# Performance work log

Hardware: AMD Instinct MI355X
Metric: run time of the kernel (lower is better)

Reference implementation:

```python
import jax, jax.numpy as jnp
import numpy as np

B, NQ, NA, C, L = 8, 2048, 64, 128, 4  # batches, queries/mol, atoms/mol, hidden, num_layers
CUTOFF = 8.0
E_AQ, E_QQ = 131072, 262144


def _ln(x, g, b):
    m = x.mean(-1, keepdims=True)
    v = ((x - m) ** 2).mean(-1, keepdims=True)
    return (x - m) * jax.lax.rsqrt(v + 1e-5) * g + b


def _egnn(p, h_src, h_tgt, pos_src, pos_tgt, t_emb, esrc, etgt):
    (mW1, mb1, mW2, mb2, cW1, cb1, cW2, cb2, nW1, nb1, nW2, nb2, g, b) = p
    rel = pos_tgt[etgt] - pos_src[esrc]                      # (E,3)
    sq = (rel ** 2).sum(-1, keepdims=True)                   # (E,1)
    mi = jnp.concatenate([h_src[esrc], h_tgt[etgt], sq, t_emb[etgt]], -1)  # (E,3C+1)
    msg = jax.nn.silu(jax.nn.silu(mi @ mW1 + mb1) @ mW2 + mb2)             # (E,C)
    w = jnp.tanh(jax.nn.silu(msg @ cW1 + cb1) @ cW2 + cb2)                 # (E,1)
    vel = jnp.zeros_like(pos_tgt).at[etgt].add(w * rel)
    agg = jnp.zeros_like(h_tgt).at[etgt].add(msg)
    u = jnp.concatenate([h_tgt, agg], -1)
    h_new = _ln(h_tgt + (jax.nn.silu(u @ nW1 + nb1) @ nW2 + nb2), g, b)
    return h_new, vel


def setup_inputs() -> dict:
    key = jax.random.key(0)
    ks = iter(jax.random.split(key, 64))
    n = lambda shape, s=0.05: jax.random.normal(next(ks), shape, dtype=jnp.float32) * s
    NQT, NAT = B * NQ, B * NA
    return dict(
        x_t=jax.random.normal(next(ks), (NQT, 3), dtype=jnp.float32) * 3.0,
        t_query=jax.random.uniform(next(ks), (NQT,), dtype=jnp.float32),
        atom_pos=jax.random.normal(next(ks), (NAT, 3), dtype=jnp.float32) * 3.0,
        atom_feat=n((NAT, 256), 1.0),
        edge_aq_src=jax.random.randint(next(ks), (E_AQ,), 0, NAT, dtype=jnp.int32),
        edge_aq_tgt=jax.random.randint(next(ks), (E_AQ,), 0, NQT, dtype=jnp.int32),
        edge_qq_src=jax.random.randint(next(ks), (E_QQ,), 0, NQT, dtype=jnp.int32),
        edge_qq_tgt=jax.random.randint(next(ks), (E_QQ,), 0, NQT, dtype=jnp.int32),
        atom_proj_W=n((256, C)), atom_proj_b=jnp.zeros((C,)),
        time_W1=n((C, 4 * C)), time_b1=jnp.zeros((4 * C,)),
        time_W2=n((4 * C, C)), time_b2=jnp.zeros((C,)),
        qi_W1=n((1, C)), qi_b1=jnp.zeros((C,)),
        qi_W2=n((C, C)), qi_b2=jnp.zeros((C,)),
        msg_W1=n((2 * L, 3 * C + 1, 2 * C)), msg_b1=jnp.zeros((2 * L, 2 * C)),
        msg_W2=n((2 * L, 2 * C, C)), msg_b2=jnp.zeros((2 * L, C)),
        cw_W1=n((2 * L, C, C // 2)), cw_b1=jnp.zeros((2 * L, C // 2)),
        cw_W2=n((2 * L, C // 2, 1)), cw_b2=jnp.zeros((2 * L, 1)),
        nu_W1=n((2 * L, 2 * C, C)), nu_b1=jnp.zeros((2 * L, C)),
        nu_W2=n((2 * L, C, C)), nu_b2=jnp.zeros((2 * L, C)),
        ln_g=jnp.ones((2 * L, C)), ln_b=jnp.zeros((2 * L, C)),
        vo_W1=n((C, C)), vo_b1=jnp.zeros((C,)),
        vo_W2=n((C, 1)), vo_b2=jnp.zeros((1,)),
    )


def reference(x_t, t_query, atom_pos, atom_feat,
              edge_aq_src, edge_aq_tgt, edge_qq_src, edge_qq_tgt,
              atom_proj_W, atom_proj_b,
              time_W1, time_b1, time_W2, time_b2,
              qi_W1, qi_b1, qi_W2, qi_b2,
              msg_W1, msg_b1, msg_W2, msg_b2,
              cw_W1, cw_b1, cw_W2, cw_b2,
              nu_W1, nu_b1, nu_W2, nu_b2,
              ln_g, ln_b,
              vo_W1, vo_b1, vo_W2, vo_b2):
    # atom features (no condition drop: eval mode)
    h_atom = atom_feat @ atom_proj_W + atom_proj_b

    # sinusoidal time embedding per query node
    half = C // 2
    freqs = jnp.exp(-np.log(10000.0) * jnp.arange(half, dtype=jnp.float32) / (half - 1))
    args = t_query[:, None] * freqs[None, :]
    emb = jnp.concatenate([jnp.sin(args), jnp.cos(args)], -1)
    t_emb = jax.nn.silu(emb @ time_W1 + time_b1) @ time_W2 + time_b2

    # init query features: log1p(mean_dist / cutoff), equal-size batches
    q = x_t.reshape(B, NQ, 3)
    a = atom_pos.reshape(B, NA, 3)
    sq = ((q[:, :, None, :] - a[:, None, :, :]) ** 2).sum(-1)  # (B,NQ,NA)
    log_dist = jnp.log1p(jnp.sqrt(sq.mean(-1)) / CUTOFF).reshape(-1, 1)
    h = jax.nn.silu(log_dist @ qi_W1 + qi_b1) @ qi_W2 + qi_b2

    layers = (msg_W1, msg_b1, msg_W2, msg_b2, cw_W1, cw_b1, cw_W2, cw_b2,
              nu_W1, nu_b1, nu_W2, nu_b2, ln_g, ln_b)
    pick = lambda j: tuple(arr[j] for arr in layers)

    vel = jnp.zeros_like(x_t)
    for i in range(L):
        h, dv = _egnn(pick(2 * i), h_atom, h, atom_pos, x_t, t_emb, edge_aq_src, edge_aq_tgt)
        vel = vel + dv
        h, dv = _egnn(pick(2 * i + 1), h, h, x_t, x_t, t_emb, edge_qq_src, edge_qq_tgt)
        vel = vel + dv

    scale = jax.nn.silu(h @ vo_W1 + vo_b1) @ vo_W2 + vo_b2   # (N_q,1)
    return vel * scale
```

## Files before the change

### kernel.cpp

```cpp
#include <hip/hip_runtime.h>

#define NQT 16384
#define NAT 512
#define EAQ 131072
#define EQQ 262144

typedef short short8 __attribute__((ext_vector_type(8)));
typedef float float4v __attribute__((ext_vector_type(4)));

__device__ __forceinline__ float silu_f(float x){ return x / (1.f + __expf(-x)); }

__device__ __forceinline__ short f2bf(float f){
  union { float f; unsigned u; } v; v.f = f;
  unsigned r = v.u + 0x7fff + ((v.u >> 16) & 1);
  return (short)(r >> 16);
}
__device__ __forceinline__ float bf2f(short s){
  union { unsigned u; float f; } v;
  v.u = ((unsigned)(unsigned short)s) << 16;
  return v.f;
}

__global__ __launch_bounds__(256) void k_hist2(
    const int* __restrict__ ta, const int* __restrict__ tq,
    int* __restrict__ ha, int* __restrict__ hq)
{
  int i = blockIdx.x*256 + threadIdx.x;
  atomicAdd(&hq[tq[i]], 1);
  if (i < EAQ) atomicAdd(&ha[ta[i]], 1);
}

__global__ __launch_bounds__(256) void k_scan2(int* __restrict__ ha, int* __restrict__ hq)
{
  int* hist = (blockIdx.x == 0) ? ha : hq;
  __shared__ int part[256];
  int t = threadIdx.x;
  int base = t * 64;
  int s = 0;
  for (int i = 0; i < 64; i++) s += hist[base + i];
  part[t] = s;
  __syncthreads();
  for (int off = 1; off < 256; off <<= 1){
    int v = (t >= off) ? part[t - off] : 0;
    __syncthreads();
    part[t] += v;
    __syncthreads();
  }
  int run = (t == 0) ? 0 : part[t-1];
  for (int i = 0; i < 64; i++){
    int h = hist[base + i];
    hist[base + i] = run;
    run += h;
  }
}

__global__ __launch_bounds__(256) void k_place2(
    const int* __restrict__ sa, const int* __restrict__ ta,
    const int* __restrict__ sq, const int* __restrict__ tq,
    int* __restrict__ ca, int* __restrict__ cq,
    int2* __restrict__ da, int2* __restrict__ dq)
{
  int i = blockIdx.x*256 + threadIdx.x;
  { int tg = tq[i]; int pos = atomicAdd(&cq[tg], 1); dq[pos] = make_int2(sq[i], tg); }
  if (i < EAQ){ int tg = ta[i]; int pos = atomicAdd(&ca[tg], 1); da[pos] = make_int2(sa[i], tg); }
}

__device__ __forceinline__ void pack_one(
    const float* __restrict__ W, short* __restrict__ out,
    int rows, int cols, int ksteps, int ntiles, int idx, int mode)
{
  int l8   = idx & 7;
  int lane = (idx >> 3) & 63;
  int kk   = (idx >> 9) % ksteps;
  int nt   = ((idx >> 9) / ksteps) % ntiles;
  int j    = idx / (512 * ksteps * ntiles);
  int k = kk*32 + (lane >> 4)*8 + l8;
  if (mode == 1) k += (k >= 256);
  else if (mode == 2) k = (k < 128) ? k + 128 : k + 129;
  int n = nt*16 + (lane & 15);
  out[idx] = f2bf(W[(size_t)j*rows*cols + (size_t)k*cols + n]);
}

__global__ __launch_bounds__(256) void k_packall(
    const float* __restrict__ mW1, const float* __restrict__ mW2,
    const float* __restrict__ cW1, const float* __restrict__ nW1,
    const float* __restrict__ nW2, const float* __restrict__ tW1,
    const float* __restrict__ tW2,
    short* W1ap, short* W1bcp, short* W2p, short* W3p,
    short* nW1p, short* nW2p, short* tW1p, short* tW2p)
{
  int b = blockIdx.x, t = threadIdx.x;
  if (b < 1024){ pack_one(mW1, W1ap, 385,256,4,16, b*256+t, 0); return; } b -= 1024;
  if (b < 2048){ pack_one(mW1, W1bcp,385,256,8,16, b*256+t, 2); return; } b -= 2048;
  if (b < 1024){ pack_one(mW2, W2p,  256,128,8, 8, b*256+t, 0); return; } b -= 1024;
  if (b <  256){ pack_one(cW1, W3p,  128, 64,4, 4, b*256+t, 0); return; } b -=  256;
  if (b < 1024){ pack_one(nW1, nW1p, 256,128,8, 8, b*256+t, 0); return; } b -= 1024;
  if (b <  512){ pack_one(nW2, nW2p, 128,128,4, 8, b*256+t, 0); return; } b -=  512;
  if (b <  256){ pack_one(tW1, tW1p, 128,512,4,32, b*256+t, 0); return; } b -=  256;
  pack_one(tW2, tW2p, 512,128,16,8, b*256+t, 0);
}

__global__ __launch_bounds__(256) void k_pre0(
    const float* __restrict__ hA, const float* __restrict__ temb,
    const float* __restrict__ mb1_0, const short* __restrict__ W1bcp0,
    const float* __restrict__ h_atom, const short* __restrict__ W1ap_base,
    short* __restrict__ Ptgt, short* __restrict__ psrc_aq)
{
  int t = threadIdx.x;
  int lane = t & 63, w = t >> 6;
  int mrow = lane & 15, quad = lane >> 4;
  int b = blockIdx.x;

  if (b < NQT/64){
    int m0 = b*64 + w*16;
    short8 areg[8];
    #pragma unroll
    for (int kk = 0; kk < 8; kk++){
      int k = kk*32 + quad*8;
      const float* bp = (kk >= 4) ? (temb + (size_t)(m0+mrow)*128 + (k - 128))
                                  : (hA   + (size_t)(m0+mrow)*128 + k);
      float4 f0 = *(const float4*)(bp);
      float4 f1 = *(const float4*)(bp + 4);
      short8 s;
      s[0]=f2bf(f0.x); s[1]=f2bf(f0.y); s[2]=f2bf(f0.z); s[3]=f2bf(f0.w);
      s[4]=f2bf(f1.x); s[5]=f2bf(f1.y); s[6]=f2bf(f1.z); s[7]=f2bf(f1.w);
      areg[kk] = s;
    }
    #pragma unroll
    for (int nt = 0; nt < 16; nt++){
      float4v acc = {0.f,0.f,0.f,0.f};
      const short8* Bb = (const short8*)(W1bcp0 + ((size_t)nt*8)*512 + lane*8);
      #pragma unroll
      for (int kk = 0; kk < 8; kk++)
        acc = __builtin_amdgcn_mfma_f32_16x16x32_bf16(areg[kk], Bb[kk*64], acc, 0, 0, 0);
      float bv = mb1_0[nt*16 + mrow];
      #pragma unroll
      for (int r = 0; r < 4; r++)
        Ptgt[(size_t)(m0 + quad*4 + r)*256 + nt*16 + mrow] = f2bf(acc[r] + bv);
    }
  } else {
    int bb = b - NQT/64;
    int idx = bb >> 3;
    int m0 = (bb & 7)*64 + w*16;
    const short* Wp = W1ap_base + (size_t)(2*idx)*32768;
    short8 areg[4];
    #pragma unroll
    for (int kk = 0; kk < 4; kk++){
      const float* bp = h_atom + (size_t)(m0+mrow)*128 + kk*32 + quad*8;
      float4 f0 = *(const float4*)(bp);
      float4 f1 = *(const float4*)(bp + 4);
      short8 s;
      s[0]=f2bf(f0.x); s[1]=f2bf(f0.y); s[2]=f2bf(f0.z); s[3]=f2bf(f0.w);
      s[4]=f2bf(f1.x); s[5]=f2bf(f1.y); s[6]=f2bf(f1.z); s[7]=f2bf(f1.w);
      areg[kk] = s;
    }
    #pragma unroll
    for (int nt = 0; nt < 16; nt++){
      float4v acc = {0.f,0.f,0.f,0.f};
      const short8* Bb = (const short8*)(Wp + ((size_t)nt*4)*512 + lane*8);
      #pragma unroll
      for (int kk = 0; kk < 4; kk++)
        acc = __builtin_amdgcn_mfma_f32_16x16x32_bf16(areg[kk], Bb[kk*64], acc, 0, 0, 0);
      #pragma unroll
      for (int r = 0; r < 4; r++)
        psrc_aq[(size_t)idx*131072 + (size_t)(m0 + quad*4 + r)*256 + nt*16 + mrow] = f2bf(acc[r]);
    }
  }
}

__global__ __launch_bounds__(128) void k_hatom(
    const float* __restrict__ feat, const float* __restrict__ W,
    const float* __restrict__ b, float* __restrict__ out)
{
  __shared__ float sf[256];
  int n = blockIdx.x, t = threadIdx.x;
  sf[t]       = feat[n*256 + t];
  sf[t + 128] = feat[n*256 + 128 + t];
  __syncthreads();
  float acc = b[t];
  for (int k = 0; k < 256; k++) acc += sf[k] * W[k*128 + t];
  out[n*128 + t] = acc;
}

__global__ __launch_bounds__(256) void k_temb(
    const float* __restrict__ tq,
    const short* __restrict__ W1p, const float* __restrict__ b1,
    const short* __restrict__ W2p, const float* __restrict__ b2,
    float* __restrict__ temb)
{
  __shared__ __align__(16) short A[32*136];
  __shared__ __align__(16) short B[32*528];
  int t = threadIdx.x;
  int n0 = blockIdx.x * 32;

  {
    int row = t >> 3, l = t & 7;
    float tv = tq[n0 + row];
    short* o = A + row*136;
    #pragma unroll
    for (int i = 0; i < 16; i++){
      int k = l*16 + i;
      int h = k & 63;
      float freq = __expf(-9.210340371976184f * (float)h * (1.f/63.f));
      float a = tv * freq;
      float v = (k < 64) ? __sinf(a) : __cosf(a);
      o[k] = f2bf(v);
    }
  }
  __syncthreads();

  int lane = t & 63, w = t >> 6;
  int mrow = lane & 15, quad = lane >> 4;

  for (int nti = 0; nti < 8; nti++){
    int nt = w*8 + nti;
    #pragma unroll
    for (int mt = 0; mt < 2; mt++){
      float4v acc = {0.f,0.f,0.f,0.f};
      const short8* Ab = (const short8*)(A + (mt*16 + mrow)*136 + quad*8);
      const short8* Bb = (const short8*)(W1p + (size_t)nt*4*512 + lane*8);
      #pragma unroll
      for (int kk = 0; kk < 4; kk++)
        acc = __builtin_amdgcn_mfma_f32_16x16x32_bf16(Ab[kk*4], Bb[kk*64], acc, 0, 0, 0);
      int n = nt*16 + mrow;
      float b1n = b1[n];
      #pragma unroll
      for (int r = 0; r < 4; r++)
        B[(mt*16 + quad*4 + r)*528 + n] = f2bf(silu_f(acc[r] + b1n));
    }
  }
  __syncthreads();

  #pragma unroll
  for (int nti = 0; nti < 2; nti++){
    int nt = w*2 + nti;
    #pragma unroll
    for (int mt = 0; mt < 2; mt++){
      float4v acc = {0.f,0.f,0.f,0.f};
      const short8* Ab = (const short8*)(B + (mt*16 + mrow)*528 + quad*8);
      const short8* Bb = (const short8*)(W2p + (size_t)nt*16*512 + lane*8);
      #pragma unroll
      for (int kk = 0; kk < 16; kk++)
        acc = __builtin_amdgcn_mfma_f32_16x16x32_bf16(Ab[kk*4], Bb[kk*64], acc, 0, 0, 0);
      int n = nt*16 + mrow;
      float b2n = b2[n];
      #pragma unroll
      for (int r = 0; r < 4; r++)
        temb[(size_t)(n0 + mt*16 + quad*4 + r)*128 + n] = acc[r] + b2n;
    }
  }
}

__global__ __launch_bounds__(128) void k_hinit(
    const float* __restrict__ x_t, const float* __restrict__ atom_pos,
    const float* __restrict__ W1, const float* __restrict__ b1,
    const float* __restrict__ W2, const float* __restrict__ b2,
    float* __restrict__ h)
{
  __shared__ float sh[128];
  __shared__ float sld;
  int n = blockIdx.x, t = threadIdx.x;
  float qx = x_t[n*3], qy = x_t[n*3+1], qz = x_t[n*3+2];
  float part = 0.f;
  if (t < 64){
    int a = (n >> 11)*64 + t;
    float dx = qx - atom_pos[a*3];
    float dy = qy - atom_pos[a*3+1];
    float dz = qz - atom_pos[a*3+2];
    part = dx*dx + dy*dy + dz*dz;
  }
  #pragma unroll
  for (int off = 32; off; off >>= 1) part += __shfl_down(part, off);
  if (t == 0) sld = log1pf(sqrtf(part * (1.f/64.f)) * 0.125f);
  __syncthreads();
  float ld = sld;
  sh[t] = silu_f(ld * W1[t] + b1[t]);
  __syncthreads();
  float acc = b2[t];
  for (int k = 0; k < 128; k++) acc += sh[k] * W2[k*128 + t];
  h[(size_t)n*128 + t] = acc;
}

__global__ __launch_bounds__(256) void k_edge(
    const short* __restrict__ Psrc, const short* __restrict__ Ptgt,
    const float* __restrict__ pos_src, const float* __restrict__ pos_tgt,
    const int2* __restrict__ sdesc,
    const float* __restrict__ w1sq,
    const short* __restrict__ W2p, const float* __restrict__ b2,
    const short* __restrict__ W3p, const float* __restrict__ b3,
    const float* __restrict__ W4,  const float* __restrict__ b4,
    float* __restrict__ agg, float* __restrict__ vel)
{
  __shared__ __align__(16) short A2[32*264];
  __shared__ __align__(16) short A3[32*136];
  __shared__ float rel_s[32*3];
  __shared__ int   tgt_s[32];
  float* msgf = (float*)A2;
  float* h3   = (float*)A2;

  int t = threadIdx.x;
  int e0 = blockIdx.x * 32;

  {
    int e = t >> 3, l = t & 7;
    int2 d = sdesc[e0 + e];
    int src = d.x, tgt = d.y;
    float rx = pos_tgt[tgt*3+0] - pos_src[src*3+0];
    float ry = pos_tgt[tgt*3+1] - pos_src[src*3+1];
    float rz = pos_tgt[tgt*3+2] - pos_src[src*3+2];
    float sqv = rx*rx + ry*ry + rz*rz;
    if (l == 0){
      rel_s[e*3+0]=rx; rel_s[e*3+1]=ry; rel_s[e*3+2]=rz;
      tgt_s[e] = tgt;
    }
    const short8* ps = (const short8*)(Psrc + (size_t)src*256);
    const short8* pt = (const short8*)(Ptgt + (size_t)tgt*256);
    #pragma unroll
    for (int c = 0; c < 4; c++){
      int ci = c*8 + l;
      int n0 = ci*8;
      short8 a = ps[ci], b = pt[ci];
      float4 w0 = *(const float4*)(w1sq + n0);
      float4 w1 = *(const float4*)(w1sq + n0 + 4);
      short8 r;
      r[0] = f2bf(silu_f(bf2f(a[0]) + bf2f(b[0]) + sqv*w0.x));
      r[1] = f2bf(silu_f(bf2f(a[1]) + bf2f(b[1]) + sqv*w0.y));
      r[2] = f2bf(silu_f(bf2f(a[2]) + bf2f(b[2]) + sqv*w0.z));
      r[3] = f2bf(silu_f(bf2f(a[3]) + bf2f(b[3]) + sqv*w0.w));
      r[4] = f2bf(silu_f(bf2f(a[4]) + bf2f(b[4]) + sqv*w1.x));
      r[5] = f2bf(silu_f(bf2f(a[5]) + bf2f(b[5]) + sqv*w1.y));
      r[6] = f2bf(silu_f(bf2f(a[6]) + bf2f(b[6]) + sqv*w1.z));
      r[7] = f2bf(silu_f(bf2f(a[7]) + bf2f(b[7]) + sqv*w1.w));
      *(short8*)(A2 + e*264 + n0) = r;
    }
  }
  __syncthreads();

  int lane = t & 63, w = t >> 6;
  int mrow = lane & 15, quad = lane >> 4;

  short8 afr[2][8];
  #pragma unroll
  for (int mt = 0; mt < 2; mt++){
    const short8* Ab = (const short8*)(A2 + (mt*16 + mrow)*264 + quad*8);
    #pragma unroll
    for (int kk = 0; kk < 8; kk++)
      afr[mt][kk] = Ab[kk*4];
  }
  float4v acc2[2][2];
  #pragma unroll
  for (int nti = 0; nti < 2; nti++){
    int nt = w*2 + nti;
    #pragma unroll
    for (int mt = 0; mt < 2; mt++){
      float4v acc = {0.f,0.f,0.f,0.f};
      const short8* Bb = (const short8*)(W2p + (size_t)nt*8*512 + lane*8);
      #pragma unroll
      for (int kk = 0; kk < 8; kk++)
        acc = __builtin_amdgcn_mfma_f32_16x16x32_bf16(afr[mt][kk], Bb[kk*64], acc, 0, 0, 0);
      acc2[nti][mt] = acc;
    }
  }
  __syncthreads();

  #pragma unroll
  for (int nti = 0; nti < 2; nti++){
    int n = (w*2 + nti)*16 + mrow;
    float b2n = b2[n];
    #pragma unroll
    for (int mt = 0; mt < 2; mt++){
      #pragma unroll
      for (int r = 0; r < 4; r++){
        int e = mt*16 + quad*4 + r;
        float v = silu_f(acc2[nti][mt][r] + b2n);
        msgf[e*132 + n] = v;
        A3[e*136 + n]   = f2bf(v);
      }
    }
  }
  __syncthreads();

  float4v acc3[2];
  {
    int nt = w;
    #pragma unroll
    for (int mt = 0; mt < 2; mt++){
      float4v acc = {0.f,0.f,0.f,0.f};
      const short8* Ab = (const short8*)(A3 + (mt*16 + mrow)*136 + quad*8);
      const short8* Bb = (const short8*)(W3p + (size_t)nt*4*512 + lane*8);
      #pragma unroll
      for (int kk = 0; kk < 4; kk++)
        acc = __builtin_amdgcn_mfma_f32_16x16x32_bf16(Ab[kk*4], Bb[kk*64], acc, 0, 0, 0);
      acc3[mt] = acc;
    }
  }

  {
    int c = t & 127, hh = t >> 7;
    int eb = hh*16;
    float run = 0.f;
    int cur = tgt_s[eb];
    for (int e = eb; e < eb + 16; e++){
      int tg = tgt_s[e];
      if (tg != cur){
        atomicAdd(&agg[(size_t)cur*128 + c], run);
        run = 0.f; cur = tg;
      }
      run += msgf[e*132 + c];
    }
    atomicAdd(&agg[(size_t)cur*128 + c], run);
  }
  __syncthreads();

  {
    int n = w*16 + mrow;
    float b3n = b3[n];
    #pragma unroll
    for (int mt = 0; mt < 2; mt++){
      #pragma unroll
      for (int r = 0; r < 4; r++){
        int e = mt*16 + quad*4 + r;
        h3[e*68 + n] = silu_f(acc3[mt][r] + b3n);
      }
    }
  }
  __syncthreads();

  {
    int e = t >> 3, l = t & 7;
    float p = 0.f;
    #pragma unroll
    for (int i = 0; i < 8; i++){
      int k = l + 8*i;
      p += h3[e*68 + k] * W4[k];
    }
    p += __shfl_xor(p, 1);
    p += __shfl_xor(p, 2);
    p += __shfl_xor(p, 4);
    if (l == 0){
      float wv = tanhf(p + b4[0]);
      int tg = tgt_s[e];
      atomicAdd(&vel[tg*3+0], wv*rel_s[e*3+0]);
      atomicAdd(&vel[tg*3+1], wv*rel_s[e*3+1]);
      atomicAdd(&vel[tg*3+2], wv*rel_s[e*3+2]);
    }
  }
}

__global__ __launch_bounds__(256) void k_node(
    const float* __restrict__ h, float* __restrict__ agg,
    const short* __restrict__ W1p, const float* __restrict__ b1,
    const short* __restrict__ W2p, const float* __restrict__ b2,
    const float* __restrict__ g, const float* __restrict__ bb_,
    float* __restrict__ h_out,
    int produce,
    const float* __restrict__ temb,
    const short* __restrict__ W1bcN, const float* __restrict__ mb1N,
    const short* __restrict__ W1aN,
    short* __restrict__ Ptgt, short* __restrict__ PsrcQ)
{
  __shared__ __align__(16) short A[32*264];
  __shared__ __align__(16) short B[32*136];
  __shared__ __align__(16) short S[32*264];
  float* r = (float*)A;
  int t = threadIdx.x;
  int n0 = blockIdx.x * 32;

  {
    int row = t >> 3, l = t & 7;
    const float4* hr = (const float4*)(h + (size_t)(n0+row)*128);
    float4*       ar = (float4*)(agg + (size_t)(n0+row)*128);
    const float4* te = (const float4*)(temb + (size_t)(n0+row)*128);
    short* o = A + row*264;
    short* so = S + row*264 + 128;
    float4 z = make_float4(0.f,0.f,0.f,0.f);
    #pragma unroll
    for (int i = 0; i < 4; i++){
      int k4 = l + 8*i;
      float4 a = hr[k4];
      o[k4*4+0]=f2bf(a.x); o[k4*4+1]=f2bf(a.y); o[k4*4+2]=f2bf(a.z); o[k4*4+3]=f2bf(a.w);
      float4 b = ar[k4];
      o[128 + k4*4+0]=f2bf(b.x); o[128 + k4*4+1]=f2bf(b.y);
      o[128 + k4*4+2]=f2bf(b.z); o[128 + k4*4+3]=f2bf(b.w);
      ar[k4] = z;
      if (produce){
        float4 c = te[k4];
        so[k4*4+0]=f2bf(c.x); so[k4*4+1]=f2bf(c.y);
        so[k4*4+2]=f2bf(c.z); so[k4*4+3]=f2bf(c.w);
      }
    }
  }
  __syncthreads();

  int lane = t & 63, w = t >> 6;
  int mrow = lane & 15, quad = lane >> 4;

  float4v accA[2][2];
  #pragma unroll
  for (int nti = 0; nti < 2; nti++){
    int nt = w*2 + nti;
    #pragma unroll
    for (int mt = 0; mt < 2; mt++){
      float4v acc = {0.f,0.f,0.f,0.f};
      const short8* Ab = (const short8*)(A + (mt*16 + mrow)*264 + quad*8);
      const short8* Bb = (const short8*)(W1p + (size_t)nt*8*512 + lane*8);
      #pragma unroll
      for (int kk = 0; kk < 8; kk++)
        acc = __builtin_amdgcn_mfma_f32_16x16x32_bf16(Ab[kk*4], Bb[kk*64], acc, 0, 0, 0);
      accA[nti][mt] = acc;
    }
  }
  __syncthreads();

  #pragma unroll
  for (int nti = 0; nti < 2; nti++){
    int n = (w*2 + nti)*16 + mrow;
    float b1n = b1[n];
    #pragma unroll
    for (int mt = 0; mt < 2; mt++){
      #pragma unroll
      for (int rr = 0; rr < 4; rr++){
        int e = mt*16 + quad*4 + rr;
        B[e*136 + n] = f2bf(silu_f(accA[nti][mt][rr] + b1n));
      }
    }
  }
  __syncthreads();

  #pragma unroll
  for (int nti = 0; nti < 2; nti++){
    int nt = w*2 + nti;
    #pragma unroll
    for (int mt = 0; mt < 2; mt++){
      float4v acc = {0.f,0.f,0.f,0.f};
      const short8* Ab = (const short8*)(B + (mt*16 + mrow)*136 + quad*8);
      const short8* Bb = (const short8*)(W2p + (size_t)nt*4*512 + lane*8);
      #pragma unroll
      for (int kk = 0; kk < 4; kk++)
        acc = __builtin_amdgcn_mfma_f32_16x16x32_bf16(Ab[kk*4], Bb[kk*64], acc, 0, 0, 0);
      int n = nt*16 + mrow;
      float b2n = b2[n];
      #pragma unroll
      for (int rr = 0; rr < 4; rr++){
        int e = mt*16 + quad*4 + rr;
        r[e*132 + n] = h[(size_t)(n0+e)*128 + n] + acc[rr] + b2n;
      }
    }
  }
  __syncthreads();

  {
    int lane2 = t & 63, wid = t >> 6;
    #pragma unroll
    for (int nn = 0; nn < 8; nn++){
      int row = wid*8 + nn;
      float a = r[row*132 + lane2], bv = r[row*132 + lane2 + 64];
      float s = a + bv, ss = a*a + bv*bv;
      #pragma unroll
      for (int off = 1; off < 64; off <<= 1){
        s  += __shfl_xor(s, off);
        ss += __shfl_xor(ss, off);
      }
      float mean = s * (1.f/128.f);
      float var  = ss * (1.f/128.f) - mean*mean;
      float rstd = rsqrtf(var + 1e-5f);
      float v0 = (a  - mean)*rstd*g[lane2]      + bb_[lane2];
      float v1 = (bv - mean)*rstd*g[lane2 + 64] + bb_[lane2 + 64];
      float* ho = h_out + (size_t)(n0+row)*128;
      ho[lane2]      = v0;
      ho[lane2 + 64] = v1;
      S[row*264 + lane2]      = f2bf(v0);
      S[row*264 + lane2 + 64] = f2bf(v1);
    }
  }
  if (!produce) return;
  __syncthreads();

  #pragma unroll
  for (int nti = 0; nti < 4; nti++){
    int nt = w*4 + nti;
    #pragma unroll
    for (int mt = 0; mt < 2; mt++){
      float4v acc = {0.f,0.f,0.f,0.f};
      const short8* Ab = (const short8*)(S + (mt*16 + mrow)*264 + quad*8);
      const short8* Bb = (const short8*)(W1bcN + (size_t)nt*8*512 + lane*8);
      #pragma unroll
      for (int kk = 0; kk < 8; kk++)
        acc = __builtin_amdgcn_mfma_f32_16x16x32_bf16(Ab[kk*4], Bb[kk*64], acc, 0, 0, 0);
      int n = nt*16 + mrow;
      float bv = mb1N[n];
      #pragma unroll
      for (int rr = 0; rr < 4; rr++)
        Ptgt[(size_t)(n0 + mt*16 + quad*4 + rr)*256 + n] = f2bf(acc[rr] + bv);
    }
  }

  if (produce == 2){
    #pragma unroll
    for (int nti = 0; nti < 4; nti++){
      int nt = w*4 + nti;
      #pragma unroll
      for (int mt = 0; mt < 2; mt++){
        float4v acc = {0.f,0.f,0.f,0.f};
        const short8* Ab = (const short8*)(S + (mt*16 + mrow)*264 + quad*8);
        const short8* Bb = (const short8*)(W1aN + (size_t)nt*4*512 + lane*8);
        #pragma unroll
        for (int kk = 0; kk < 4; kk++)
          acc = __builtin_amdgcn_mfma_f32_16x16x32_bf16(Ab[kk*4], Bb[kk*64], acc, 0, 0, 0);
        int n = nt*16 + mrow;
        #pragma unroll
        for (int rr = 0; rr < 4; rr++)
          PsrcQ[(size_t)(n0 + mt*16 + quad*4 + rr)*256 + n] = f2bf(acc[rr]);
      }
    }
  }
}

__global__ __launch_bounds__(128) void k_out(
    const float* __restrict__ h, const float* __restrict__ vel,
    const float* __restrict__ W1, const float* __restrict__ b1,
    const float* __restrict__ W2, const float* __restrict__ b2,
    float* __restrict__ out)
{
  __shared__ float sh[128];
  __shared__ float spart[2];
  int n = blockIdx.x, t = threadIdx.x;
  sh[t] = h[(size_t)n*128 + t];
  __syncthreads();
  float acc = b1[t];
  for (int k = 0; k < 128; k++) acc += sh[k] * W1[k*128 + t];
  float p = silu_f(acc) * W2[t];
  #pragma unroll
  for (int off = 32; off; off >>= 1) p += __shfl_down(p, off);
  if ((t & 63) == 0) spart[t >> 6] = p;
  __syncthreads();
  if (t < 3){
    float scale = spart[0] + spart[1] + b2[0];
    out[n*3 + t] = vel[n*3 + t] * scale;
  }
}

extern "C" void kernel_launch(void* const* d_in, const int* in_sizes, int n_in,
                              void* d_out, int out_size, void* d_ws, size_t ws_size,
                              hipStream_t stream)
{
  const float* x_t       = (const float*)d_in[0];
  const float* t_query   = (const float*)d_in[1];
  const float* atom_pos  = (const float*)d_in[2];
  const float* atom_feat = (const float*)d_in[3];
  const int*   e_aq_s = (const int*)d_in[4];
  const int*   e_aq_t = (const int*)d_in[5];
  const int*   e_qq_s = (const int*)d_in[6];
  const int*   e_qq_t = (const int*)d_in[7];
  const float* apW  = (const float*)d_in[8];
  const float* apb  = (const float*)d_in[9];
  const float* tW1  = (const float*)d_in[10];
  const float* tb1  = (const float*)d_in[11];
  const float* tW2  = (const float*)d_in[12];
  const float* tb2  = (const float*)d_in[13];
  const float* qiW1 = (const float*)d_in[14];
  const float* qib1 = (const float*)d_in[15];
  const float* qiW2 = (const float*)d_in[16];
  const float* qib2 = (const float*)d_in[17];
  const float* mW1  = (const float*)d_in[18];
  const float* mb1  = (const float*)d_in[19];
  const float* mW2  = (const float*)d_in[20];
  const float* mb2  = (const float*)d_in[21];
  const float* cW1  = (const float*)d_in[22];
  const float* cb1  = (const float*)d_in[23];
  const float* cW2  = (const float*)d_in[24];
  const float* cb2  = (const float*)d_in[25];
  const float* nW1  = (const float*)d_in[26];
  const float* nb1  = (const float*)d_in[27];
  const float* nW2  = (const float*)d_in[28];
  const float* nb2  = (const float*)d_in[29];
  const float* lng  = (const float*)d_in[30];
  const float* lnb  = (const float*)d_in[31];
  const float* voW1 = (const float*)d_in[32];
  const float* vob1 = (const float*)d_in[33];
  const float* voW2 = (const float*)d_in[34];
  const float* vob2 = (const float*)d_in[35];
  float* out = (float*)d_out;

  float* ws     = (float*)d_ws;
  float* h_atom = ws;
  float* temb   = h_atom + 65536;
  float* hA     = temb + 2097152;
  float* hB     = hA + 2097152;
  float* agg    = hB + 2097152;
  float* vel    = agg + 2097152;
  short* W1ap   = (short*)(vel + 49152);
  short* W1bcp  = W1ap + 262144;
  short* W2p    = W1bcp + 524288;
  short* W3p    = W2p + 262144;
  short* nW1p   = W3p + 65536;
  short* nW2p   = nW1p + 262144;
  short* tW1p   = nW2p + 131072;
  short* tW2p   = tW1p + 65536;
  short* PsrcQ  = tW2p + 65536;
  short* Ptgt   = PsrcQ + 4194304;
  short* psrc_aq= Ptgt + 4194304;
  int*   hist_a = (int*)(psrc_aq + 524288);
  int*   hist_q = hist_a + 16384;
  int2*  desc_a = (int2*)(hist_q + 16384);
  int2*  desc_q = desc_a + EAQ;

  hipMemsetAsync(hist_a, 0, 2*16384*sizeof(int), stream);
  k_hist2<<<EQQ/256, 256, 0, stream>>>(e_aq_t, e_qq_t, hist_a, hist_q);
  k_scan2<<<2, 256, 0, stream>>>(hist_a, hist_q);
  k_place2<<<EQQ/256, 256, 0, stream>>>(e_aq_s, e_aq_t, e_qq_s, e_qq_t,
                                        hist_a, hist_q, desc_a, desc_q);

  k_packall<<<6400, 256, 0, stream>>>(mW1, mW2, cW1, nW1, nW2, tW1, tW2,
      W1ap, W1bcp, W2p, W3p, nW1p, nW2p, tW1p, tW2p);

  hipMemsetAsync(agg, 0, (size_t)(NQT*128 + NQT*3)*sizeof(float), stream);
  k_hatom<<<NAT, 128, 0, stream>>>(atom_feat, apW, apb, h_atom);
  k_temb<<<NQT/32, 256, 0, stream>>>(t_query, tW1p, tb1, tW2p, tb2, temb);
  k_hinit<<<NQT, 128, 0, stream>>>(x_t, atom_pos, qiW1, qib1, qiW2, qib2, hA);

  k_pre0<<<NQT/64 + 32, 256, 0, stream>>>(hA, temb, mb1, W1bcp, h_atom, W1ap,
                                          Ptgt, psrc_aq);

  float* hc = hA; float* hn = hB;
  for (int j = 0; j < 8; j++){
    int half = j & 1;
    const int2* dsc = half ? desc_q : desc_a;
    int E = half ? EQQ : EAQ;
    const short* psrc = half ? PsrcQ : (psrc_aq + (size_t)(j >> 1)*131072);

    k_edge<<<E/32, 256, 0, stream>>>(psrc, Ptgt,
        half ? x_t : atom_pos, x_t, dsc,
        mW1 + (size_t)j*385*256 + 65536,
        W2p + (size_t)j*32768, mb2 + (size_t)j*128,
        W3p + (size_t)j*8192,  cb1 + (size_t)j*64,
        cW2 + (size_t)j*64,    cb2 + (size_t)j,
        agg, vel);

    int jn = (j < 7) ? (j + 1) : 7;
    int produce = (j == 7) ? 0 : ((half == 0) ? 2 : 1);
    k_node<<<NQT/32, 256, 0, stream>>>(hc, agg,
        nW1p + (size_t)j*32768, nb1 + (size_t)j*128,
        nW2p + (size_t)j*16384, nb2 + (size_t)j*128,
        lng + (size_t)j*128,    lnb + (size_t)j*128, hn,
        produce, temb,
        W1bcp + (size_t)jn*65536, mb1 + (size_t)jn*256,
        W1ap + (size_t)jn*32768,
        Ptgt, PsrcQ);
    float* tmp = hc; hc = hn; hn = tmp;
  }
  k_out<<<NQT, 128, 0, stream>>>(hc, vel, voW1, vob1, voW2, vob2, out);
}
```

Measured before the change: 1.295 ms.

## Keep target projection in fp32 and batch 16 nodes per block in hinit/out

The per-target precomputed projection Ptgt is now stored as fp32 instead of bf16. This removes a rounding step but doubles the gathered bytes per edge in k_edge. Separately, k_hinit and k_out now process 16 nodes per 256-thread block instead of one node per 128-thread block. This amortizes the weight reads and cuts the block count, at the cost of each thread doing 8 output columns serially. The Ptgt change looks like an accuracy fix that adds memory traffic, while the node batching targets launch and weight-load overhead.

```diff
diff --git a/kernel.cpp b/kernel.cpp
--- a/kernel.cpp
+++ b/kernel.cpp
@@ -104,7 +104,7 @@
     const float* __restrict__ hA, const float* __restrict__ temb,
     const float* __restrict__ mb1_0, const short* __restrict__ W1bcp0,
     const float* __restrict__ h_atom, const short* __restrict__ W1ap_base,
-    short* __restrict__ Ptgt, short* __restrict__ psrc_aq)
+    float* __restrict__ Ptgt, short* __restrict__ psrc_aq)
 {
   int t = threadIdx.x;
   int lane = t & 63, w = t >> 6;
@@ -136,7 +136,7 @@
       float bv = mb1_0[nt*16 + mrow];
       #pragma unroll
       for (int r = 0; r < 4; r++)
-        Ptgt[(size_t)(m0 + quad*4 + r)*256 + nt*16 + mrow] = f2bf(acc[r] + bv);
+        Ptgt[(size_t)(m0 + quad*4 + r)*256 + nt*16 + mrow] = acc[r] + bv;
     }
   } else {
     int bb = b - NQT/64;
@@ -251,38 +251,52 @@
   }
 }
 
-__global__ __launch_bounds__(128) void k_hinit(
+__global__ __launch_bounds__(256) void k_hinit(
     const float* __restrict__ x_t, const float* __restrict__ atom_pos,
     const float* __restrict__ W1, const float* __restrict__ b1,
     const float* __restrict__ W2, const float* __restrict__ b2,
     float* __restrict__ h)
 {
-  __shared__ float sh[128];
-  __shared__ float sld;
-  int n = blockIdx.x, t = threadIdx.x;
+  __shared__ float sh[16*128];
+  int t = threadIdx.x;
+  int n0 = blockIdx.x * 16;
+  int r = t >> 4, l = t & 15;
+  int n = n0 + r;
+
   float qx = x_t[n*3], qy = x_t[n*3+1], qz = x_t[n*3+2];
+  int batch = n >> 11;
   float part = 0.f;
-  if (t < 64){
-    int a = (n >> 11)*64 + t;
-    float dx = qx - atom_pos[a*3];
-    float dy = qy - atom_pos[a*3+1];
-    float dz = qz - atom_pos[a*3+2];
-    part = dx*dx + dy*dy + dz*dz;
-  }
-  #pragma unroll
-  for (int off = 32; off; off >>= 1) part += __shfl_down(part, off);
-  if (t == 0) sld = log1pf(sqrtf(part * (1.f/64.f)) * 0.125f);
-  __syncthreads();
-  float ld = sld;
-  sh[t] = silu_f(ld * W1[t] + b1[t]);
-  __syncthreads();
-  float acc = b2[t];
-  for (int k = 0; k < 128; k++) acc += sh[k] * W2[k*128 + t];
-  h[(size_t)n*128 + t] = acc;
+  #pragma unroll
+  for (int i = 0; i < 4; i++){
+    int a = batch*64 + l*4 + i;
+    float dx = qx - atom_pos[a*3], dy = qy - atom_pos[a*3+1], dz = qz - atom_pos[a*3+2];
+    part += dx*dx + dy*dy + dz*dz;
+  }
+  part += __shfl_xor(part, 1);
+  part += __shfl_xor(part, 2);
+  part += __shfl_xor(part, 4);
+  part += __shfl_xor(part, 8);
+  float ld = log1pf(sqrtf(part * (1.f/64.f)) * 0.125f);
+
+  #pragma unroll
+  for (int cc = 0; cc < 8; cc++){
+    int c = l*8 + cc;
+    sh[r*128 + c] = silu_f(ld * W1[c] + b1[c]);
+  }
+  __syncthreads();
+
+  const float* shr = sh + r*128;
+  #pragma unroll
+  for (int cc = 0; cc < 8; cc++){
+    int c = l*8 + cc;
+    float acc = b2[c];
+    for (int k = 0; k < 128; k++) acc += shr[k] * W2[k*128 + c];
+    h[(size_t)n*128 + c] = acc;
+  }
 }
 
 __global__ __launch_bounds__(256) void k_edge(
-    const short* __restrict__ Psrc, const short* __restrict__ Ptgt,
+    const short* __restrict__ Psrc, const float* __restrict__ Ptgt,
     const float* __restrict__ pos_src, const float* __restrict__ pos_tgt,
     const int2* __restrict__ sdesc,
     const float* __restrict__ w1sq,
@@ -313,24 +327,25 @@
       rel_s[e*3+0]=rx; rel_s[e*3+1]=ry; rel_s[e*3+2]=rz;
       tgt_s[e] = tgt;
     }
-    const short8* ps = (const short8*)(Psrc + (size_t)src*256);
-    const short8* pt = (const short8*)(Ptgt + (size_t)tgt*256);
+    const short8*  ps = (const short8*)(Psrc + (size_t)src*256);
+    const float4*  pt = (const float4*)(Ptgt + (size_t)tgt*256);
     #pragma unroll
     for (int c = 0; c < 4; c++){
       int ci = c*8 + l;
       int n0 = ci*8;
-      short8 a = ps[ci], b = pt[ci];
+      short8 a = ps[ci];
+      float4 b0 = pt[ci*2], b1v = pt[ci*2+1];
       float4 w0 = *(const float4*)(w1sq + n0);
       float4 w1 = *(const float4*)(w1sq + n0 + 4);
       short8 r;
-      r[0] = f2bf(silu_f(bf2f(a[0]) + bf2f(b[0]) + sqv*w0.x));
-      r[1] = f2bf(silu_f(bf2f(a[1]) + bf2f(b[1]) + sqv*w0.y));
-      r[2] = f2bf(silu_f(bf2f(a[2]) + bf2f(b[2]) + sqv*w0.z));
-      r[3] = f2bf(silu_f(bf2f(a[3]) + bf2f(b[3]) + sqv*w0.w));
-      r[4] = f2bf(silu_f(bf2f(a[4]) + bf2f(b[4]) + sqv*w1.x));
-      r[5] = f2bf(silu_f(bf2f(a[5]) + bf2f(b[5]) + sqv*w1.y));
-      r[6] = f2bf(silu_f(bf2f(a[6]) + bf2f(b[6]) + sqv*w1.z));
-      r[7] = f2bf(silu_f(bf2f(a[7]) + bf2f(b[7]) + sqv*w1.w));
+      r[0] = f2bf(silu_f(bf2f(a[0]) + b0.x  + sqv*w0.x));
+      r[1] = f2bf(silu_f(bf2f(a[1]) + b0.y  + sqv*w0.y));
+      r[2] = f2bf(silu_f(bf2f(a[2]) + b0.z  + sqv*w0.z));
+      r[3] = f2bf(silu_f(bf2f(a[3]) + b0.w  + sqv*w0.w));
+      r[4] = f2bf(silu_f(bf2f(a[4]) + b1v.x + sqv*w1.x));
+      r[5] = f2bf(silu_f(bf2f(a[5]) + b1v.y + sqv*w1.y));
+      r[6] = f2bf(silu_f(bf2f(a[6]) + b1v.z + sqv*w1.z));
+      r[7] = f2bf(silu_f(bf2f(a[7]) + b1v.w + sqv*w1.w));
       *(short8*)(A2 + e*264 + n0) = r;
     }
   }
@@ -457,7 +472,7 @@
     const float* __restrict__ temb,
     const short* __restrict__ W1bcN, const float* __restrict__ mb1N,
     const short* __restrict__ W1aN,
-    short* __restrict__ Ptgt, short* __restrict__ PsrcQ)
+    float* __restrict__ Ptgt, short* __restrict__ PsrcQ)
 {
   __shared__ __align__(16) short A[32*264];
   __shared__ __align__(16) short B[32*136];
@@ -591,7 +606,7 @@
       float bv = mb1N[n];
       #pragma unroll
       for (int rr = 0; rr < 4; rr++)
-        Ptgt[(size_t)(n0 + mt*16 + quad*4 + rr)*256 + n] = f2bf(acc[rr] + bv);
+        Ptgt[(size_t)(n0 + mt*16 + quad*4 + rr)*256 + n] = acc[rr] + bv;
     }
   }
 
@@ -616,27 +631,45 @@
   }
 }
 
-__global__ __launch_bounds__(128) void k_out(
+__global__ __launch_bounds__(256) void k_out(
     const float* __restrict__ h, const float* __restrict__ vel,
     const float* __restrict__ W1, const float* __restrict__ b1,
     const float* __restrict__ W2, const float* __restrict__ b2,
     float* __restrict__ out)
 {
-  __shared__ float sh[128];
-  __shared__ float spart[2];
-  int n = blockIdx.x, t = threadIdx.x;
-  sh[t] = h[(size_t)n*128 + t];
-  __syncthreads();
-  float acc = b1[t];
-  for (int k = 0; k < 128; k++) acc += sh[k] * W1[k*128 + t];
-  float p = silu_f(acc) * W2[t];
-  #pragma unroll
-  for (int off = 32; off; off >>= 1) p += __shfl_down(p, off);
-  if ((t & 63) == 0) spart[t >> 6] = p;
-  __syncthreads();
-  if (t < 3){
-    float scale = spart[0] + spart[1] + b2[0];
-    out[n*3 + t] = vel[n*3 + t] * scale;
+  __shared__ float sh[16*128];
+  __shared__ float sc[16];
+  int t = threadIdx.x;
+  int n0 = blockIdx.x * 16;
+  int r = t >> 4, l = t & 15;
+
+  {
+    const float4* src = (const float4*)(h + (size_t)(n0 + r)*128);
+    float4* dst = (float4*)(sh + r*128);
+    dst[l*2]   = src[l*2];
+    dst[l*2+1] = src[l*2+1];
+  }
+  __syncthreads();
+
+  const float* hr = sh + r*128;
+  float part = 0.f;
+  #pragma unroll
+  for (int cc = 0; cc < 8; cc++){
+    int c = l*8 + cc;
+    float acc = b1[c];
+    for (int k = 0; k < 128; k++) acc += hr[k] * W1[k*128 + c];
+    part += silu_f(acc) * W2[c];
+  }
+  part += __shfl_xor(part, 1);
+  part += __shfl_xor(part, 2);
+  part += __shfl_xor(part, 4);
+  part += __shfl_xor(part, 8);
+  if (l == 0) sc[r] = part + b2[0];
+  __syncthreads();
+
+  if (t < 48){
+    int rr = t / 3, d = t % 3;
+    out[(size_t)(n0+rr)*3 + d] = vel[(size_t)(n0+rr)*3 + d] * sc[rr];
   }
 }
 
@@ -698,9 +731,9 @@
   short* tW1p   = nW2p + 131072;
   short* tW2p   = tW1p + 65536;
   short* PsrcQ  = tW2p + 65536;
-  short* Ptgt   = PsrcQ + 4194304;
-  short* psrc_aq= Ptgt + 4194304;
-  int*   hist_a = (int*)(psrc_aq + 524288);
+  short* psrc_aq= PsrcQ + 4194304;
+  float* PtgtF  = (float*)(psrc_aq + 524288);
+  int*   hist_a = (int*)(PtgtF + 4194304);
   int*   hist_q = hist_a + 16384;
   int2*  desc_a = (int2*)(hist_q + 16384);
   int2*  desc_q = desc_a + EAQ;
@@ -717,10 +750,10 @@
   hipMemsetAsync(agg, 0, (size_t)(NQT*128 + NQT*3)*sizeof(float), stream);
   k_hatom<<<NAT, 128, 0, stream>>>(atom_feat, apW, apb, h_atom);
   k_temb<<<NQT/32, 256, 0, stream>>>(t_query, tW1p, tb1, tW2p, tb2, temb);
-  k_hinit<<<NQT, 128, 0, stream>>>(x_t, atom_pos, qiW1, qib1, qiW2, qib2, hA);
+  k_hinit<<<NQT/16, 256, 0, stream>>>(x_t, atom_pos, qiW1, qib1, qiW2, qib2, hA);
 
   k_pre0<<<NQT/64 + 32, 256, 0, stream>>>(hA, temb, mb1, W1bcp, h_atom, W1ap,
-                                          Ptgt, psrc_aq);
+                                          PtgtF, psrc_aq);
 
   float* hc = hA; float* hn = hB;
   for (int j = 0; j < 8; j++){
@@ -729,7 +762,7 @@
     int E = half ? EQQ : EAQ;
     const short* psrc = half ? PsrcQ : (psrc_aq + (size_t)(j >> 1)*131072);
 
-    k_edge<<<E/32, 256, 0, stream>>>(psrc, Ptgt,
+    k_edge<<<E/32, 256, 0, stream>>>(psrc, PtgtF,
         half ? x_t : atom_pos, x_t, dsc,
         mW1 + (size_t)j*385*256 + 65536,
         W2p + (size_t)j*32768, mb2 + (size_t)j*128,
@@ -746,8 +779,8 @@
         produce, temb,
         W1bcp + (size_t)jn*65536, mb1 + (size_t)jn*256,
         W1ap + (size_t)jn*32768,
-        Ptgt, PsrcQ);
+        PtgtF, PsrcQ);
     float* tmp = hc; hc = hn; hn = tmp;
   }
-  k_out<<<NQT, 128, 0, stream>>>(hc, vel, voW1, vob1, voW2, vob2, out);
-}
+  k_out<<<NQT/16, 256, 0, stream>>>(hc, vel, voW1, vob1, voW2, vob2, out);
+}
```

After: 2.174 ms. 67.9% more time.
